# Kernel tuning notes

Measured on AMD Instinct MI355X. Metric: run time of the kernel, lower is better.

The kernel has to match this reference:

```python
import jax, jax.numpy as jnp
import numpy as np


def setup_inputs() -> dict:
    key = jax.random.key(0)
    ks = jax.random.split(key, 5)
    B, S, H, F, E = 2, 2048, 768, 1536, 8
    scale_h = 1.0 / np.sqrt(H)
    scale_f = 1.0 / np.sqrt(F)
    return {
        "hidden_states": jax.random.normal(ks[0], (B, S, H), dtype=jnp.float32),
        "gate_w": jax.random.normal(ks[1], (E, H), dtype=jnp.float32) * scale_h,
        "w1": jax.random.normal(ks[2], (E, F, H), dtype=jnp.float32) * scale_h,
        "w3": jax.random.normal(ks[3], (E, F, H), dtype=jnp.float32) * scale_h,
        "w2": jax.random.normal(ks[4], (E, H, F), dtype=jnp.float32) * scale_f,
        "k": 2,
    }


def reference(hidden_states, gate_w, w1, w3, w2, k):
    B, S, H = hidden_states.shape
    E = gate_w.shape[0]
    x = hidden_states.reshape(-1, H)                     # [T, H]
    T = x.shape[0]

    # Router: softmax in fp32, top-k, renormalize among selected experts.
    router_logits = x @ gate_w.T                         # [T, E]
    probs = jax.nn.softmax(router_logits.astype(jnp.float32), axis=-1)
    top_w, top_i = jax.lax.top_k(probs, k)               # [T, k]
    top_w = top_w / jnp.sum(top_w, axis=-1, keepdims=True)
    top_w = top_w.astype(x.dtype)

    # Scatter top-k weights into dense [T, E] combine weights (0 for unselected).
    combine = jnp.zeros((T, E), dtype=x.dtype)
    combine = combine.at[jnp.arange(T)[:, None], top_i].set(top_w)

    # SwiGLU experts (zero-weight experts contribute exactly 0 to the sum).
    g = jnp.einsum("th,efh->tef", x, w1)                 # [T, E, F]
    u = jnp.einsum("th,efh->tef", x, w3)                 # [T, E, F]
    act = jax.nn.silu(g) * u                             # [T, E, F]
    expert_out = jnp.einsum("tef,ehf->teh", act, w2)     # [T, E, H]
    y = jnp.einsum("te,teh->th", combine, expert_out)    # [T, H]

    return y.reshape(B, S, H), router_logits
```

## Files before the change

### kernel.cpp

```cpp
#include <hip/hip_runtime.h>
#include <hip/hip_bf16.h>

#define T_TOK 4096
#define H_DIM 768
#define E_NUM 8
#define F_DIM 1536

typedef __bf16 bf16x8 __attribute__((ext_vector_type(8)));
typedef float f32x4 __attribute__((ext_vector_type(4)));
typedef unsigned int u32;

#define VMCNT(n) asm volatile("s_waitcnt vmcnt(" #n ")" ::: "memory")
#define CFENCE() asm volatile("" ::: "memory")

__device__ __forceinline__ unsigned short f2bf(float f) {
    unsigned int u = __float_as_uint(f);
    u += 0x7FFF + ((u >> 16) & 1);
    return (unsigned short)(u >> 16);
}

__device__ __forceinline__ void gload16(const unsigned short* g, unsigned short* l) {
    __builtin_amdgcn_global_load_lds(
        (const __attribute__((address_space(1))) u32*)(g),
        (__attribute__((address_space(3))) u32*)(l),
        16, 0, 0);
}

__global__ void convert_bf16_kernel(const float* __restrict__ src,
                                    unsigned short* __restrict__ dst, int n) {
    int i = (blockIdx.x * blockDim.x + threadIdx.x) * 4;
    int stride = gridDim.x * blockDim.x * 4;
    for (; i < n; i += stride) {
        float4 v = *reinterpret_cast<const float4*>(src + i);
        ushort4 o;
        o.x = f2bf(v.x); o.y = f2bf(v.y); o.z = f2bf(v.z); o.w = f2bf(v.w);
        *reinterpret_cast<ushort4*>(dst + i) = o;
    }
}

__global__ __launch_bounds__(256) void router_kernel(
    const float* __restrict__ x,
    const float* __restrict__ gw,
    float* __restrict__ logits_out,
    float* __restrict__ weight,
    int* __restrict__ eidx,
    unsigned short* __restrict__ xb) {
    int t = blockIdx.x * 4 + (threadIdx.x >> 6);
    int lane = threadIdx.x & 63;

    const float4* xr = reinterpret_cast<const float4*>(x + (size_t)t * H_DIM);
    float4 xv[3];
#pragma unroll
    for (int i = 0; i < 3; ++i) xv[i] = xr[i * 64 + lane];

    unsigned short* xbr = xb + (size_t)t * H_DIM;
#pragma unroll
    for (int i = 0; i < 3; ++i) {
        ushort4 o;
        o.x = f2bf(xv[i].x); o.y = f2bf(xv[i].y);
        o.z = f2bf(xv[i].z); o.w = f2bf(xv[i].w);
        *reinterpret_cast<ushort4*>(xbr + (i * 64 + lane) * 4) = o;
    }

    float v[E_NUM];
#pragma unroll
    for (int e = 0; e < E_NUM; ++e) {
        const float4* g = reinterpret_cast<const float4*>(gw + e * H_DIM);
        float p = 0.f;
#pragma unroll
        for (int i = 0; i < 3; ++i) {
            float4 gv = g[i * 64 + lane];
            p += xv[i].x * gv.x + xv[i].y * gv.y + xv[i].z * gv.z + xv[i].w * gv.w;
        }
        v[e] = p;
    }
#pragma unroll
    for (int d = 1; d < 8; d <<= 1)
#pragma unroll
        for (int e = 0; e < E_NUM; ++e) v[e] += __shfl_xor(v[e], d);
    int me = lane & 7;
    float le = v[0];
#pragma unroll
    for (int e = 1; e < E_NUM; ++e) le = (me == e) ? v[e] : le;
#pragma unroll
    for (int d = 8; d < 64; d <<= 1) le += __shfl_xor(le, d);

    if (lane < 8) logits_out[t * E_NUM + lane] = le;

    float m0 = le;
#pragma unroll
    for (int d = 1; d < 8; d <<= 1) m0 = fmaxf(m0, __shfl_xor(m0, d));
    unsigned long long b0 = __ballot(le == m0);
    int e0 = (__ffsll((long long)b0) - 1) & 7;
    float le1 = (me == e0) ? -3.4e38f : le;
    float m1 = le1;
#pragma unroll
    for (int d = 1; d < 8; d <<= 1) m1 = fmaxf(m1, __shfl_xor(m1, d));
    unsigned long long b1 = __ballot(le1 == m1);
    int e1 = (__ffsll((long long)b1) - 1) & 7;

    if (lane == 0) {
        float w0 = 1.f / (1.f + __expf(m1 - m0));
        weight[t * 2 + 0] = w0;
        weight[t * 2 + 1] = 1.f - w0;
        eidx[t] = e0 | (e1 << 8);
    }
}

__global__ __launch_bounds__(256) void build_lists_kernel(
    const int* __restrict__ eidx,
    int* __restrict__ list,
    int* __restrict__ counts) {
    int e = blockIdx.x;
    int tid = threadIdx.x;
    int lane = tid & 63;
    int wv = tid >> 6;
    __shared__ int wsum[4];
    __shared__ int wbase[4];
    __shared__ int sbase;
    if (tid == 0) sbase = 0;
    __syncthreads();
    for (int c = 0; c < T_TOK; c += 256) {
        int tok = c + tid;
        int pk = eidx[tok];
        int slot = -1;
        if ((pk & 255) == e) slot = tok * 2;
        else if ((pk >> 8) == e) slot = tok * 2 + 1;
        unsigned long long m = __ballot(slot >= 0);
        int prefix = __popcll(m & ((1ull << lane) - 1ull));
        if (lane == 0) wsum[wv] = __popcll(m);
        __syncthreads();
        if (tid == 0) {
            int s = sbase;
#pragma unroll
            for (int i = 0; i < 4; ++i) { wbase[i] = s; s += wsum[i]; }
            sbase = s;
        }
        __syncthreads();
        if (slot >= 0) list[e * T_TOK + wbase[wv] + prefix] = slot;
        __syncthreads();
    }
    if (tid == 0) counts[e] = sbase;
}

__global__ __launch_bounds__(256, 3) void gemm13_kernel(
    const unsigned short* __restrict__ xb,
    const unsigned short* __restrict__ w1b,
    const unsigned short* __restrict__ w3b,
    const int* __restrict__ list,
    const int* __restrict__ counts,
    unsigned short* __restrict__ act) {
    int orig = blockIdx.x;
    int wg = (orig & 7) * 768 + (orig >> 3);
    int tm = wg & 31;
    int tn = (wg >> 5) % 24;
    int e = wg / (32 * 24);

    int cnt = counts[e];
    if (tm * 128 >= cnt) return;
    const int* lst = list + e * T_TOK + tm * 128;
    int mrem = cnt - tm * 128;

    __shared__ unsigned short sA[2][128 * 32];
    __shared__ unsigned short sB1[2][64 * 32];
    __shared__ unsigned short sB3[2][64 * 32];

    int tid = threadIdx.x;
    int lane = tid & 63;
    int wid = tid >> 6;

    int r0 = tid >> 2;
    int r1 = r0 + 64;
    int c8 = ((tid & 3) ^ ((r0 >> 1) & 3)) * 8;
    int tok0 = lst[(r0 < mrem) ? r0 : 0] >> 1;
    int tok1 = lst[(r1 < mrem) ? r1 : 0] >> 1;
    const unsigned short* gA0 = xb + (size_t)tok0 * H_DIM + c8;
    const unsigned short* gA1 = xb + (size_t)tok1 * H_DIM + c8;
    const unsigned short* gB1 = w1b + ((size_t)e * F_DIM + tn * 64 + r0) * H_DIM + c8;
    const unsigned short* gB3 = w3b + ((size_t)e * F_DIM + tn * 64 + r0) * H_DIM + c8;

    auto stage = [&](int b, int kt) {
        gload16(gA0 + kt, &sA[b][wid * 512]);
        gload16(gA1 + kt, &sA[b][2048 + wid * 512]);
        gload16(gB1 + kt, &sB1[b][wid * 512]);
        gload16(gB3 + kt, &sB3[b][wid * 512]);
    };

    int wr = (wid >> 1) * 64;
    int wc = (wid & 1) * 32;
    int fr = lane & 15;
    int kb = ((lane >> 4) ^ ((lane >> 1) & 3)) * 8;

    f32x4 accG[4][2] = {};
    f32x4 accU[4][2] = {};

    stage(0, 0);
    __syncthreads();
    int buf = 0;
    for (int kt = 0; kt < H_DIM; kt += 32) {
        if (kt + 32 < H_DIM) {
            stage(buf ^ 1, kt + 32);
            VMCNT(4);
        } else {
            VMCNT(0);
        }
        __builtin_amdgcn_s_barrier();
        CFENCE();

        bf16x8 a[4], b1[2], b3[2];
#pragma unroll
        for (int mi = 0; mi < 4; ++mi)
            a[mi] = *reinterpret_cast<const bf16x8*>(&sA[buf][(wr + mi * 16 + fr) * 32 + kb]);
#pragma unroll
        for (int ni = 0; ni < 2; ++ni) {
            b1[ni] = *reinterpret_cast<const bf16x8*>(&sB1[buf][(wc + ni * 16 + fr) * 32 + kb]);
            b3[ni] = *reinterpret_cast<const bf16x8*>(&sB3[buf][(wc + ni * 16 + fr) * 32 + kb]);
        }
#pragma unroll
        for (int mi = 0; mi < 4; ++mi)
#pragma unroll
            for (int ni = 0; ni < 2; ++ni) {
                accG[mi][ni] = __builtin_amdgcn_mfma_f32_16x16x32_bf16(a[mi], b1[ni], accG[mi][ni], 0, 0, 0);
                accU[mi][ni] = __builtin_amdgcn_mfma_f32_16x16x32_bf16(a[mi], b3[ni], accU[mi][ni], 0, 0, 0);
            }
        CFENCE();
        __builtin_amdgcn_s_barrier();
        buf ^= 1;
    }

    int rg = (lane >> 4) * 4;
    int ci = lane & 15;
#pragma unroll
    for (int mi = 0; mi < 4; ++mi) {
#pragma unroll
        for (int r = 0; r < 4; ++r) {
            int m = wr + mi * 16 + rg + r;
            if (m >= mrem) continue;
            int entry = lst[m];
            size_t rowOff = (size_t)entry * F_DIM + tn * 64;
#pragma unroll
            for (int ni = 0; ni < 2; ++ni) {
                float g = accG[mi][ni][r];
                float u = accU[mi][ni][r];
                float s = g / (1.f + __expf(-g));
                act[rowOff + wc + ni * 16 + ci] = f2bf(s * u);
            }
        }
    }
}

__global__ __launch_bounds__(256, 4) void gemm2_kernel(
    const unsigned short* __restrict__ act,
    const unsigned short* __restrict__ w2b,
    const int* __restrict__ list,
    const int* __restrict__ counts,
    const float* __restrict__ weight,
    float* __restrict__ ybuf) {
    int orig = blockIdx.x;
    int wg = (orig & 7) * 384 + (orig >> 3);
    int tm = wg & 31;
    int tn = (wg >> 5) % 12;
    int e = wg / (32 * 12);

    int cnt = counts[e];
    if (tm * 128 >= cnt) return;
    const int* lst = list + e * T_TOK + tm * 128;
    int mrem = cnt - tm * 128;

    __shared__ unsigned short sA[2][128 * 32];
    __shared__ unsigned short sB[2][64 * 32];

    int tid = threadIdx.x;
    int lane = tid & 63;
    int wid = tid >> 6;

    int r0 = tid >> 2;
    int r1 = r0 + 64;
    int c8 = ((tid & 3) ^ ((r0 >> 1) & 3)) * 8;
    int row0 = lst[(r0 < mrem) ? r0 : 0];
    int row1 = lst[(r1 < mrem) ? r1 : 0];
    const unsigned short* gA0 = act + (size_t)row0 * F_DIM + c8;
    const unsigned short* gA1 = act + (size_t)row1 * F_DIM + c8;
    const unsigned short* gB = w2b + ((size_t)e * H_DIM + tn * 64 + r0) * F_DIM + c8;

    auto stage = [&](int b, int kt) {
        gload16(gA0 + kt, &sA[b][wid * 512]);
        gload16(gA1 + kt, &sA[b][2048 + wid * 512]);
        gload16(gB + kt, &sB[b][wid * 512]);
    };

    int wr = (wid >> 1) * 64;
    int wc = (wid & 1) * 32;
    int fr = lane & 15;
    int kb = ((lane >> 4) ^ ((lane >> 1) & 3)) * 8;

    f32x4 acc[4][2] = {};

    stage(0, 0);
    __syncthreads();
    int buf = 0;
    for (int kt = 0; kt < F_DIM; kt += 32) {
        if (kt + 32 < F_DIM) {
            stage(buf ^ 1, kt + 32);
            VMCNT(3);
        } else {
            VMCNT(0);
        }
        __builtin_amdgcn_s_barrier();
        CFENCE();

        bf16x8 a[4], b[2];
#pragma unroll
        for (int mi = 0; mi < 4; ++mi)
            a[mi] = *reinterpret_cast<const bf16x8*>(&sA[buf][(wr + mi * 16 + fr) * 32 + kb]);
#pragma unroll
        for (int ni = 0; ni < 2; ++ni)
            b[ni] = *reinterpret_cast<const bf16x8*>(&sB[buf][(wc + ni * 16 + fr) * 32 + kb]);
#pragma unroll
        for (int mi = 0; mi < 4; ++mi)
#pragma unroll
            for (int ni = 0; ni < 2; ++ni)
                acc[mi][ni] = __builtin_amdgcn_mfma_f32_16x16x32_bf16(a[mi], b[ni], acc[mi][ni], 0, 0, 0);
        CFENCE();
        __builtin_amdgcn_s_barrier();
        buf ^= 1;
    }

    int rg = (lane >> 4) * 4;
    int ci = lane & 15;
#pragma unroll
    for (int mi = 0; mi < 4; ++mi) {
#pragma unroll
        for (int r = 0; r < 4; ++r) {
            int m = wr + mi * 16 + rg + r;
            if (m >= mrem) continue;
            int entry = lst[m];
            float wv = weight[entry];
            size_t rowOff = (size_t)entry * H_DIM + tn * 64;
#pragma unroll
            for (int ni = 0; ni < 2; ++ni)
                ybuf[rowOff + wc + ni * 16 + ci] = acc[mi][ni][r] * wv;
        }
    }
}

__global__ void combine_kernel(const float* __restrict__ ybuf, float* __restrict__ y) {
    int v = blockIdx.x * blockDim.x + threadIdx.x;
    if (v >= T_TOK * H_DIM / 4) return;
    int t = v / (H_DIM / 4);
    int hv = v % (H_DIM / 4);
    float4 a = reinterpret_cast<const float4*>(ybuf + (size_t)(2 * t) * H_DIM)[hv];
    float4 b = reinterpret_cast<const float4*>(ybuf + (size_t)(2 * t + 1) * H_DIM)[hv];
    float4 r;
    r.x = a.x + b.x; r.y = a.y + b.y; r.z = a.z + b.z; r.w = a.w + b.w;
    reinterpret_cast<float4*>(y)[v] = r;
}

extern "C" void kernel_launch(void* const* d_in, const int* in_sizes, int n_in,
                              void* d_out, int out_size, void* d_ws, size_t ws_size,
                              hipStream_t stream) {
    const float* x  = (const float*)d_in[0];
    const float* gw = (const float*)d_in[1];
    const float* w1 = (const float*)d_in[2];
    const float* w3 = (const float*)d_in[3];
    const float* w2 = (const float*)d_in[4];

    float* y = (float*)d_out;
    float* logits_out = y + (size_t)T_TOK * H_DIM;

    char* ws = (char*)d_ws;
    size_t off = 0;
    auto alloc = [&](size_t bytes) -> char* {
        char* p = ws + off;
        off += (bytes + 255) & ~(size_t)255;
        return p;
    };
    unsigned short* xb  = (unsigned short*)alloc((size_t)T_TOK * H_DIM * 2);
    unsigned short* w1b = (unsigned short*)alloc((size_t)E_NUM * F_DIM * H_DIM * 2);
    unsigned short* w3b = (unsigned short*)alloc((size_t)E_NUM * F_DIM * H_DIM * 2);
    unsigned short* w2b = (unsigned short*)alloc((size_t)E_NUM * H_DIM * F_DIM * 2);
    unsigned short* act = (unsigned short*)alloc((size_t)T_TOK * 2 * F_DIM * 2);
    float* ybuf   = (float*)alloc((size_t)T_TOK * 2 * H_DIM * 4);
    float* weight = (float*)alloc((size_t)T_TOK * 2 * 4);
    int* list     = (int*)alloc((size_t)E_NUM * T_TOK * 4);
    int* counts   = (int*)alloc((size_t)E_NUM * 4);
    int* eidx     = (int*)alloc((size_t)T_TOK * 4);

    convert_bf16_kernel<<<2048, 256, 0, stream>>>(w1, w1b, E_NUM * F_DIM * H_DIM);
    convert_bf16_kernel<<<2048, 256, 0, stream>>>(w3, w3b, E_NUM * F_DIM * H_DIM);
    convert_bf16_kernel<<<2048, 256, 0, stream>>>(w2, w2b, E_NUM * H_DIM * F_DIM);

    router_kernel<<<T_TOK / 4, 256, 0, stream>>>(x, gw, logits_out, weight, eidx, xb);

    build_lists_kernel<<<E_NUM, 256, 0, stream>>>(eidx, list, counts);

    gemm13_kernel<<<6144, 256, 0, stream>>>(xb, w1b, w3b, list, counts, act);

    gemm2_kernel<<<3072, 256, 0, stream>>>(act, w2b, list, counts, weight, ybuf);

    combine_kernel<<<(T_TOK * H_DIM / 4 + 255) / 256, 256, 0, stream>>>(ybuf, y);
}
```

Before: 175.8 us.

## Triple-buffer LDS in expert GEMMs and merge weight conversions into one kernel

Both expert GEMM kernels now use a three-stage LDS ring buffer that prefetches two K-tiles ahead, with vmcnt waits adjusted to match, so global loads have more time to land before they are needed. The three separate fp32-to-bf16 weight conversion launches are replaced by one kernel that covers all three weight tensors, removing two launches. The extra stage raises LDS use per block (from about 32KB to 48KB in gemm13), which may cut how many blocks fit on a CU given the launch bounds. The merged conversion kernel also adds an integer divide and a select per element.

After: 176.8 us. No clear change (+0.5%).

```diff
diff --git a/kernel.cpp b/kernel.cpp
--- a/kernel.cpp
+++ b/kernel.cpp
@@ -5,6 +5,7 @@
 #define H_DIM 768
 #define E_NUM 8
 #define F_DIM 1536
+#define WELEM (E_NUM * F_DIM * H_DIM)
 
 typedef __bf16 bf16x8 __attribute__((ext_vector_type(8)));
 typedef float f32x4 __attribute__((ext_vector_type(4)));
@@ -26,15 +27,23 @@
         16, 0, 0);
 }
 
-__global__ void convert_bf16_kernel(const float* __restrict__ src,
-                                    unsigned short* __restrict__ dst, int n) {
+__global__ void convert3_kernel(const float* __restrict__ s0,
+                                const float* __restrict__ s1,
+                                const float* __restrict__ s2,
+                                unsigned short* __restrict__ d0,
+                                unsigned short* __restrict__ d1,
+                                unsigned short* __restrict__ d2) {
     int i = (blockIdx.x * blockDim.x + threadIdx.x) * 4;
     int stride = gridDim.x * blockDim.x * 4;
-    for (; i < n; i += stride) {
-        float4 v = *reinterpret_cast<const float4*>(src + i);
+    for (; i < 3 * WELEM; i += stride) {
+        int r = i / WELEM;
+        int j = i - r * WELEM;
+        const float* s = (r == 0) ? s0 : (r == 1) ? s1 : s2;
+        unsigned short* d = (r == 0) ? d0 : (r == 1) ? d1 : d2;
+        float4 v = *reinterpret_cast<const float4*>(s + j);
         ushort4 o;
         o.x = f2bf(v.x); o.y = f2bf(v.y); o.z = f2bf(v.z); o.w = f2bf(v.w);
-        *reinterpret_cast<ushort4*>(dst + i) = o;
+        *reinterpret_cast<ushort4*>(d + j) = o;
     }
 }
 
@@ -161,9 +170,9 @@
     const int* lst = list + e * T_TOK + tm * 128;
     int mrem = cnt - tm * 128;
 
-    __shared__ unsigned short sA[2][128 * 32];
-    __shared__ unsigned short sB1[2][64 * 32];
-    __shared__ unsigned short sB3[2][64 * 32];
+    __shared__ unsigned short sA[3][128 * 32];
+    __shared__ unsigned short sB1[3][64 * 32];
+    __shared__ unsigned short sB3[3][64 * 32];
 
     int tid = threadIdx.x;
     int lane = tid & 63;
@@ -194,12 +203,16 @@
     f32x4 accG[4][2] = {};
     f32x4 accU[4][2] = {};
 
+    const int NT = H_DIM / 32;
     stage(0, 0);
-    __syncthreads();
-    int buf = 0;
-    for (int kt = 0; kt < H_DIM; kt += 32) {
-        if (kt + 32 < H_DIM) {
-            stage(buf ^ 1, kt + 32);
+    stage(1, 32);
+    int cur = 0;
+    for (int t = 0; t < NT; ++t) {
+        if (t + 2 < NT) {
+            int nb = cur + 2; if (nb >= 3) nb -= 3;
+            stage(nb, (t + 2) * 32);
+            VMCNT(8);
+        } else if (t + 1 < NT) {
             VMCNT(4);
         } else {
             VMCNT(0);
@@ -210,11 +223,11 @@
         bf16x8 a[4], b1[2], b3[2];
 #pragma unroll
         for (int mi = 0; mi < 4; ++mi)
-            a[mi] = *reinterpret_cast<const bf16x8*>(&sA[buf][(wr + mi * 16 + fr) * 32 + kb]);
+            a[mi] = *reinterpret_cast<const bf16x8*>(&sA[cur][(wr + mi * 16 + fr) * 32 + kb]);
 #pragma unroll
         for (int ni = 0; ni < 2; ++ni) {
-            b1[ni] = *reinterpret_cast<const bf16x8*>(&sB1[buf][(wc + ni * 16 + fr) * 32 + kb]);
-            b3[ni] = *reinterpret_cast<const bf16x8*>(&sB3[buf][(wc + ni * 16 + fr) * 32 + kb]);
+            b1[ni] = *reinterpret_cast<const bf16x8*>(&sB1[cur][(wc + ni * 16 + fr) * 32 + kb]);
+            b3[ni] = *reinterpret_cast<const bf16x8*>(&sB3[cur][(wc + ni * 16 + fr) * 32 + kb]);
         }
 #pragma unroll
         for (int mi = 0; mi < 4; ++mi)
@@ -225,7 +238,7 @@
             }
         CFENCE();
         __builtin_amdgcn_s_barrier();
-        buf ^= 1;
+        cur = (cur + 1 < 3) ? cur + 1 : 0;
     }
 
     int rg = (lane >> 4) * 4;
@@ -267,8 +280,8 @@
     const int* lst = list + e * T_TOK + tm * 128;
     int mrem = cnt - tm * 128;
 
-    __shared__ unsigned short sA[2][128 * 32];
-    __shared__ unsigned short sB[2][64 * 32];
+    __shared__ unsigned short sA[3][128 * 32];
+    __shared__ unsigned short sB[3][64 * 32];
 
     int tid = threadIdx.x;
     int lane = tid & 63;
@@ -296,12 +309,16 @@
 
     f32x4 acc[4][2] = {};
 
+    const int NT = F_DIM / 32;
     stage(0, 0);
-    __syncthreads();
-    int buf = 0;
-    for (int kt = 0; kt < F_DIM; kt += 32) {
-        if (kt + 32 < F_DIM) {
-            stage(buf ^ 1, kt + 32);
+    stage(1, 32);
+    int cur = 0;
+    for (int t = 0; t < NT; ++t) {
+        if (t + 2 < NT) {
+            int nb = cur + 2; if (nb >= 3) nb -= 3;
+            stage(nb, (t + 2) * 32);
+            VMCNT(6);
+        } else if (t + 1 < NT) {
             VMCNT(3);
         } else {
             VMCNT(0);
@@ -312,10 +329,10 @@
         bf16x8 a[4], b[2];
 #pragma unroll
         for (int mi = 0; mi < 4; ++mi)
-            a[mi] = *reinterpret_cast<const bf16x8*>(&sA[buf][(wr + mi * 16 + fr) * 32 + kb]);
+            a[mi] = *reinterpret_cast<const bf16x8*>(&sA[cur][(wr + mi * 16 + fr) * 32 + kb]);
 #pragma unroll
         for (int ni = 0; ni < 2; ++ni)
-            b[ni] = *reinterpret_cast<const bf16x8*>(&sB[buf][(wc + ni * 16 + fr) * 32 + kb]);
+            b[ni] = *reinterpret_cast<const bf16x8*>(&sB[cur][(wc + ni * 16 + fr) * 32 + kb]);
 #pragma unroll
         for (int mi = 0; mi < 4; ++mi)
 #pragma unroll
@@ -323,7 +340,7 @@
                 acc[mi][ni] = __builtin_amdgcn_mfma_f32_16x16x32_bf16(a[mi], b[ni], acc[mi][ni], 0, 0, 0);
         CFENCE();
         __builtin_amdgcn_s_barrier();
-        buf ^= 1;
+        cur = (cur + 1 < 3) ? cur + 1 : 0;
     }
 
     int rg = (lane >> 4) * 4;
@@ -376,9 +393,9 @@
         return p;
     };
     unsigned short* xb  = (unsigned short*)alloc((size_t)T_TOK * H_DIM * 2);
-    unsigned short* w1b = (unsigned short*)alloc((size_t)E_NUM * F_DIM * H_DIM * 2);
-    unsigned short* w3b = (unsigned short*)alloc((size_t)E_NUM * F_DIM * H_DIM * 2);
-    unsigned short* w2b = (unsigned short*)alloc((size_t)E_NUM * H_DIM * F_DIM * 2);
+    unsigned short* w1b = (unsigned short*)alloc((size_t)WELEM * 2);
+    unsigned short* w3b = (unsigned short*)alloc((size_t)WELEM * 2);
+    unsigned short* w2b = (unsigned short*)alloc((size_t)WELEM * 2);
     unsigned short* act = (unsigned short*)alloc((size_t)T_TOK * 2 * F_DIM * 2);
     float* ybuf   = (float*)alloc((size_t)T_TOK * 2 * H_DIM * 4);
     float* weight = (float*)alloc((size_t)T_TOK * 2 * 4);
@@ -386,9 +403,7 @@
     int* counts   = (int*)alloc((size_t)E_NUM * 4);
     int* eidx     = (int*)alloc((size_t)T_TOK * 4);
 
-    convert_bf16_kernel<<<2048, 256, 0, stream>>>(w1, w1b, E_NUM * F_DIM * H_DIM);
-    convert_bf16_kernel<<<2048, 256, 0, stream>>>(w3, w3b, E_NUM * F_DIM * H_DIM);
-    convert_bf16_kernel<<<2048, 256, 0, stream>>>(w2, w2b, E_NUM * H_DIM * F_DIM);
+    convert3_kernel<<<4096, 256, 0, stream>>>(w1, w3, w2, w1b, w3b, w2b);
 
     router_kernel<<<T_TOK / 4, 256, 0, stream>>>(x, gw, logits_out, weight, eidx, xb);
 
```
